# Optimization experiments

Measured on AMD Instinct MI355X. Metric: run time of the kernel, lower is better.

The kernel has to match this reference:

```python
import jax, jax.numpy as jnp
import numpy as np

HEIGHT = 32
SIGMA = 2.0
NUM_NEGATIVE = 4096
N, C = 32, 512
L = HEIGHT * HEIGHT


def _grid_weight(height: int, sigma: float) -> jnp.ndarray:
    # distance_weights: pairwise Euclidean distance between grid points
    ii, jj = np.meshgrid(np.arange(height), np.arange(height), indexing='ij')
    coords = np.stack([ii.ravel(), jj.ravel()], axis=1).astype(np.float32)  # [L, 2]
    d2 = ((coords[:, None, :] - coords[None, :, :]) ** 2).sum(-1)  # squared dist [L, L]
    w = -(0.5 / sigma ** 2) * d2
    np.fill_diagonal(w, -np.inf)
    return jax.nn.softmax(jnp.asarray(w, dtype=jnp.float32), axis=1)


def setup_inputs() -> dict:
    key = jax.random.key(0)
    k1, k2 = jax.random.split(key)
    embedding = jax.random.normal(k1, (N, L, C), dtype=jnp.float32)
    weight = _grid_weight(HEIGHT, SIGMA)  # [L, L] softmax-normalized grid kernel
    neg_indices = jax.random.randint(k2, (NUM_NEGATIVE,), 0, N * L, dtype=jnp.int64)
    return {"embedding": embedding, "weight": weight, "neg_indices": neg_indices}


def reference(embedding, weight, neg_indices):
    n, l, c = embedding.shape
    # F.normalize(dim=-1), eps=1e-12
    norm = jnp.maximum(jnp.linalg.norm(embedding, axis=-1, keepdims=True), 1e-12)
    e = embedding / norm  # [N, L, C]
    # target = weight @ e  (broadcast over batch)
    target = jnp.einsum('kl,nlc->nkc', weight, e)  # [N, L, C]
    sim_pos = jnp.sum(e * target, axis=-1)  # [N, L]
    flat = e.reshape(-1, c)  # [N*L, C]
    negatives = flat[neg_indices]  # [M, C]
    sim_neg = jnp.einsum('nlc,mc->nlm', e, negatives)  # [N, L, M]
    logits = jnp.concatenate([sim_pos[..., None], sim_neg], axis=2).reshape(n * l, 1 + neg_indices.shape[0])
    # CrossEntropyLoss with target class 0, mean reduction
    loss = -jnp.mean(jax.nn.log_softmax(logits, axis=-1)[:, 0])
    return loss
```

## Files before the change

kernel.cpp:

```cpp
#include <hip/hip_runtime.h>
#include <hip/hip_bf16.h>
#include <stdint.h>

#define L_DIM 1024
#define C_DIM 512
#define CB4 256
#define N_BATCH 32
#define M_NEG 4096
#define NROWS (N_BATCH * L_DIM)

typedef float f32x4 __attribute__((ext_vector_type(4)));
typedef int i32x4 __attribute__((ext_vector_type(4)));
typedef int i32x8 __attribute__((ext_vector_type(8)));

#define E4_SCALE 32.0f
#define MX_SCALE 122
#define FMT_FP4 4

template <int GOFF>
__device__ __forceinline__ void gl_lds16(const uint8_t* g, uint8_t* l) {
  __builtin_amdgcn_global_load_lds(
      (const __attribute__((address_space(1))) void*)g,
      (__attribute__((address_space(3))) void*)l, 16, GOFF, 0);
}

__device__ __forceinline__ uint32_t fp4_enc(float x) {
  const uint32_t s = (__float_as_uint(x) >> 31) << 3;
  const float a = fabsf(x);
  uint32_t c;
  c = a < 0.25f ? 0u
    : a < 0.75f ? 1u
    : a < 1.25f ? 2u
    : a < 1.75f ? 3u
    : a < 2.5f  ? 4u
    : a < 3.5f  ? 5u
    : a < 5.0f  ? 6u : 7u;
  return s | c;
}

__device__ __forceinline__ i32x8 fp4_op(i32x4 d) {
  return __builtin_shufflevector(d, d, 0, 1, 2, 3, -1, -1, -1, -1);
}

__device__ __forceinline__ int swz(int row) { return (row >> 1) & 3; }

__global__ __launch_bounds__(256) void k_normalize(const float* __restrict__ emb,
                                                   uint8_t* __restrict__ out,
                                                   float* __restrict__ zerobuf,
                                                   float* __restrict__ loss_out) {
  if (blockIdx.x < 1152) zerobuf[blockIdx.x * 256 + threadIdx.x] = 0.0f;
  if (blockIdx.x == 0 && threadIdx.x == 0) loss_out[0] = 0.0f;
  const int lane = threadIdx.x & 63;
  const int wave = threadIdx.x >> 6;
  const long row = (long)blockIdx.x * 4 + wave;
  const float4* src = (const float4*)(emb + row * C_DIM);
  float4 v0 = src[2 * lane];
  float4 v1 = src[2 * lane + 1];
  float ss = v0.x * v0.x + v0.y * v0.y + v0.z * v0.z + v0.w * v0.w +
             v1.x * v1.x + v1.y * v1.y + v1.z * v1.z + v1.w * v1.w;
#pragma unroll
  for (int off = 1; off < 64; off <<= 1) ss += __shfl_xor(ss, off, 64);
  const float s = E4_SCALE / fmaxf(sqrtf(ss), 1e-12f);
  uint32_t pk = fp4_enc(v0.x * s)        | (fp4_enc(v0.y * s) << 4) |
                (fp4_enc(v0.z * s) << 8) | (fp4_enc(v0.w * s) << 12) |
                (fp4_enc(v1.x * s) << 16)| (fp4_enc(v1.y * s) << 20) |
                (fp4_enc(v1.z * s) << 24)| (fp4_enc(v1.w * s) << 28);
  ((uint32_t*)(out + row * CB4))[lane] = pk;
}

__global__ __launch_bounds__(256, 4) void k_gemm_fused(
    const uint8_t* __restrict__ E4, const int* __restrict__ idx,
    const float* __restrict__ W, float* __restrict__ rowsum8,
    float* __restrict__ simpos) {
  __shared__ __align__(16) unsigned char smem_raw[40960];

  const int tid = threadIdx.x;
  const int lane = tid & 63;
  const int wave = tid >> 6;
  const int wm = wave >> 1, wn = wave & 1;
  const int q = lane >> 4, c16 = lane & 15;

  const int bid = blockIdx.x;

  if (bid < 1024) {
    uint8_t* sN = (uint8_t*)smem_raw;
    uint8_t* sE = sN + 32768;
    const int xcd = bid & 7, slot = bid >> 3;
    const long negBase = (long)(slot & 31) * 128;
    const long eBase0 = (long)(xcd * 4 + (slot >> 5)) * 1024;
    float* myrs = rowsum8 + (long)xcd * NROWS;

    const uint8_t* pN[2];
#pragma unroll
    for (int r = 0; r < 2; ++r) {
      const int c = r * 256 + tid;
      const int rw = c >> 2, cb = c & 3;
      pN[r] = E4 + (long)idx[negBase + rw] * CB4 + (cb ^ swz(rw)) * 16;
    }
    gl_lds16<0>(pN[0], sN + tid * 16);
    gl_lds16<0>(pN[1], sN + (256 + tid) * 16);
    gl_lds16<64>(pN[0], sN + 8192 + tid * 16);
    gl_lds16<64>(pN[1], sN + 8192 + (256 + tid) * 16);
    gl_lds16<128>(pN[0], sN + 16384 + tid * 16);
    gl_lds16<128>(pN[1], sN + 16384 + (256 + tid) * 16);
    gl_lds16<192>(pN[0], sN + 24576 + tid * 16);
    gl_lds16<192>(pN[1], sN + 24576 + (256 + tid) * 16);

    const uint8_t* pE[2];
#pragma unroll
    for (int r = 0; r < 2; ++r) {
      const int c = r * 256 + tid;
      const int rw = c >> 2, cb = c & 3;
      pE[r] = E4 + (eBase0 + rw) * CB4 + (cb ^ swz(rw)) * 16;
    }

    int ldsN[4], ldsE[4];
#pragma unroll
    for (int j = 0; j < 4; ++j) {
      const int rowN = wm * 64 + j * 16 + c16;
      ldsN[j] = rowN * 64 + (q ^ swz(rowN)) * 16;
      const int rowE = wn * 64 + j * 16 + c16;
      ldsE[j] = rowE * 64 + (q ^ swz(rowE)) * 16;
    }

    for (int et = 0; et < 8; ++et) {
      f32x4 acc[4][4] = {};
      auto kstep = [&](int ks) {
        __syncthreads();
        i32x8 efr[4];
#pragma unroll
        for (int j = 0; j < 4; ++j)
          efr[j] = fp4_op(*(const i32x4*)(sE + ldsE[j]));
#pragma unroll
        for (int i = 0; i < 4; ++i) {
          i32x8 nf = fp4_op(*(const i32x4*)(sN + ks * 8192 + ldsN[i]));
#pragma unroll
          for (int j = 0; j < 4; ++j)
            acc[i][j] = __builtin_amdgcn_mfma_scale_f32_16x16x128_f8f6f4(
                nf, efr[j], acc[i][j], FMT_FP4, FMT_FP4,
                0, MX_SCALE, 0, MX_SCALE);
        }
        __syncthreads();
      };
      gl_lds16<0>(pE[0], sE + tid * 16);
      gl_lds16<0>(pE[1], sE + (256 + tid) * 16);
      kstep(0);
      gl_lds16<64>(pE[0], sE + tid * 16);
      gl_lds16<64>(pE[1], sE + (256 + tid) * 16);
      kstep(1);
      gl_lds16<128>(pE[0], sE + tid * 16);
      gl_lds16<128>(pE[1], sE + (256 + tid) * 16);
      kstep(2);
      gl_lds16<192>(pE[0], sE + tid * 16);
      gl_lds16<192>(pE[1], sE + (256 + tid) * 16);
      kstep(3);
      pE[0] += 32768;
      pE[1] += 32768;

      const long eCol = eBase0 + (long)et * 128 + wn * 64 + c16;
#pragma unroll
      for (int j = 0; j < 4; ++j) {
        float s = 0.0f;
#pragma unroll
        for (int i = 0; i < 4; ++i)
#pragma unroll
          for (int r = 0; r < 4; ++r) s += __expf(acc[i][j][r]);
        s += __shfl_xor(s, 16, 64);
        s += __shfl_xor(s, 32, 64);
        if (q == 0) atomicAdd(&myrs[eCol + j * 16], s);
      }
    }
  } else {
    uint8_t* sA = (uint8_t*)smem_raw;
    uint8_t* sB = sA + 8192;
    const int t = bid - 1024;
    const int xcd = t & 7, slot = t >> 3;
    const long n = xcd * 4 + (slot & 3);
    const int inner = slot >> 2;
    const long rowBase = (long)(inner & 7) * 128;
    const long colBase = (long)(inner >> 3) * 128;
    const long aBase = n * L_DIM + rowBase;

    const uint8_t* pA[2];
    const uint8_t* pB[2];
#pragma unroll
    for (int r = 0; r < 2; ++r) {
      const int c = r * 256 + tid;
      const int rw = c >> 2, cb = c & 3;
      pA[r] = E4 + (aBase + rw) * CB4 + (cb ^ swz(rw)) * 16;
      pB[r] = E4 + (n * L_DIM + colBase + rw) * CB4 + (cb ^ swz(rw)) * 16;
    }
    int ldsB[4], ldsA[4];
#pragma unroll
    for (int j = 0; j < 4; ++j) {
      const int rowB = wn * 64 + j * 16 + c16;
      ldsB[j] = rowB * 64 + (q ^ swz(rowB)) * 16;
      const int rowA = wm * 64 + j * 16 + c16;
      ldsA[j] = rowA * 64 + (q ^ swz(rowA)) * 16;
    }

    f32x4 acc[4][4] = {};
    auto kstep = [&]() {
      __syncthreads();
      i32x8 bfr[4];
#pragma unroll
      for (int j = 0; j < 4; ++j)
        bfr[j] = fp4_op(*(const i32x4*)(sB + ldsB[j]));
#pragma unroll
      for (int i = 0; i < 4; ++i) {
        i32x8 af = fp4_op(*(const i32x4*)(sA + ldsA[i]));
#pragma unroll
        for (int j = 0; j < 4; ++j)
          acc[i][j] = __builtin_amdgcn_mfma_scale_f32_16x16x128_f8f6f4(
              af, bfr[j], acc[i][j], FMT_FP4, FMT_FP4,
              0, MX_SCALE, 0, MX_SCALE);
      }
      __syncthreads();
    };
    gl_lds16<0>(pA[0], sA + tid * 16);
    gl_lds16<0>(pA[1], sA + (256 + tid) * 16);
    gl_lds16<0>(pB[0], sB + tid * 16);
    gl_lds16<0>(pB[1], sB + (256 + tid) * 16);
    kstep();
    gl_lds16<64>(pA[0], sA + tid * 16);
    gl_lds16<64>(pA[1], sA + (256 + tid) * 16);
    gl_lds16<64>(pB[0], sB + tid * 16);
    gl_lds16<64>(pB[1], sB + (256 + tid) * 16);
    kstep();
    gl_lds16<128>(pA[0], sA + tid * 16);
    gl_lds16<128>(pA[1], sA + (256 + tid) * 16);
    gl_lds16<128>(pB[0], sB + tid * 16);
    gl_lds16<128>(pB[1], sB + (256 + tid) * 16);
    kstep();
    gl_lds16<192>(pA[0], sA + tid * 16);
    gl_lds16<192>(pA[1], sA + (256 + tid) * 16);
    gl_lds16<192>(pB[0], sB + tid * 16);
    gl_lds16<192>(pB[1], sB + (256 + tid) * 16);
    kstep();

    float* G = (float*)smem_raw;
#pragma unroll
    for (int p = 0; p < 4; ++p) {
      if (wm == (p >> 1)) {
#pragma unroll
        for (int ii = 0; ii < 2; ++ii) {
          const int i = (p & 1) * 2 + ii;
#pragma unroll
          for (int j = 0; j < 4; ++j)
#pragma unroll
            for (int r = 0; r < 4; ++r)
              G[(ii * 16 + q * 4 + r) * 132 + wn * 64 + j * 16 + c16] =
                  acc[i][j][r];
        }
      }
      __syncthreads();
      {
        const int rr = tid >> 3;
        const int chunk = tid & 7;
        const long krow = rowBase + p * 32 + rr;
        float v = 0.0f;
#pragma unroll
        for (int u = 0; u < 4; ++u) {
          const float4 g = *(const float4*)(G + rr * 132 + chunk * 16 + u * 4);
          const float4 w4 = *(const float4*)(W + krow * L_DIM + colBase +
                                             chunk * 16 + u * 4);
          v += g.x * w4.x + g.y * w4.y + g.z * w4.z + g.w * w4.w;
        }
        v += __shfl_xor(v, 1, 64);
        v += __shfl_xor(v, 2, 64);
        v += __shfl_xor(v, 4, 64);
        if (chunk == 0) atomicAdd(&simpos[n * L_DIM + krow], v);
      }
      __syncthreads();
    }
  }
}

__global__ __launch_bounds__(256) void k_finalize(const float* __restrict__ rowsum8,
                                                  const float* __restrict__ simpos,
                                                  float* __restrict__ out) {
  const int gid = blockIdx.x * 256 + threadIdx.x;
  float rs = 0.0f;
#pragma unroll
  for (int x = 0; x < 8; ++x) rs += rowsum8[x * NROWS + gid];
  const float sp = simpos[gid];
  float v = __logf(rs + __expf(sp)) - sp;
#pragma unroll
  for (int off = 1; off < 64; off <<= 1) v += __shfl_xor(v, off, 64);
  __shared__ float ws[4];
  if ((threadIdx.x & 63) == 0) ws[threadIdx.x >> 6] = v;
  __syncthreads();
  if (threadIdx.x == 0)
    atomicAdd(out, (ws[0] + ws[1] + ws[2] + ws[3]) * (1.0f / (float)NROWS));
}

extern "C" void kernel_launch(void* const* d_in, const int* in_sizes, int n_in,
                              void* d_out, int out_size, void* d_ws, size_t ws_size,
                              hipStream_t stream) {
  const float* emb = (const float*)d_in[0];
  const float* weight = (const float*)d_in[1];
  const int* negidx = (const int*)d_in[2];
  float* out = (float*)d_out;
  char* ws = (char*)d_ws;

  uint8_t* E4 = (uint8_t*)ws;
  float* rowsum8 = (float*)(ws + 8388608);
  float* simpos = (float*)(ws + 9437184);

  k_normalize<<<NROWS / 4, 256, 0, stream>>>(emb, E4, rowsum8, out);
  k_gemm_fused<<<3072, 256, 0, stream>>>(E4, negidx, weight, rowsum8, simpos);
  k_finalize<<<NROWS / 256, 256, 0, stream>>>(rowsum8, simpos, out);
}
```

Measured before the change: 190.6 us.

## Swap stationary operand in negative GEMM and reduce row sums in registers

After: 176.8 us. -7.2%, faster.

```diff
diff --git a/kernel.cpp b/kernel.cpp
--- a/kernel.cpp
+++ b/kernel.cpp
@@ -46,9 +46,9 @@
 
 __global__ __launch_bounds__(256) void k_normalize(const float* __restrict__ emb,
                                                    uint8_t* __restrict__ out,
-                                                   float* __restrict__ zerobuf,
+                                                   float* __restrict__ simpos,
                                                    float* __restrict__ loss_out) {
-  if (blockIdx.x < 1152) zerobuf[blockIdx.x * 256 + threadIdx.x] = 0.0f;
+  if (blockIdx.x < 128) simpos[blockIdx.x * 256 + threadIdx.x] = 0.0f;
   if (blockIdx.x == 0 && threadIdx.x == 0) loss_out[0] = 0.0f;
   const int lane = threadIdx.x & 63;
   const int wave = threadIdx.x >> 6;
@@ -70,7 +70,7 @@
 
 __global__ __launch_bounds__(256, 4) void k_gemm_fused(
     const uint8_t* __restrict__ E4, const int* __restrict__ idx,
-    const float* __restrict__ W, float* __restrict__ rowsum8,
+    const float* __restrict__ W, float* __restrict__ rowsum4,
     float* __restrict__ simpos) {
   __shared__ __align__(16) unsigned char smem_raw[40960];
 
@@ -83,92 +83,119 @@
   const int bid = blockIdx.x;
 
   if (bid < 1024) {
-    uint8_t* sN = (uint8_t*)smem_raw;
-    uint8_t* sE = sN + 32768;
-    const int xcd = bid & 7, slot = bid >> 3;
-    const long negBase = (long)(slot & 31) * 128;
-    const long eBase0 = (long)(xcd * 4 + (slot >> 5)) * 1024;
-    float* myrs = rowsum8 + (long)xcd * NROWS;
-
-    const uint8_t* pN[2];
-#pragma unroll
-    for (int r = 0; r < 2; ++r) {
-      const int c = r * 256 + tid;
-      const int rw = c >> 2, cb = c & 3;
-      pN[r] = E4 + (long)idx[negBase + rw] * CB4 + (cb ^ swz(rw)) * 16;
-    }
-    gl_lds16<0>(pN[0], sN + tid * 16);
-    gl_lds16<0>(pN[1], sN + (256 + tid) * 16);
-    gl_lds16<64>(pN[0], sN + 8192 + tid * 16);
-    gl_lds16<64>(pN[1], sN + 8192 + (256 + tid) * 16);
-    gl_lds16<128>(pN[0], sN + 16384 + tid * 16);
-    gl_lds16<128>(pN[1], sN + 16384 + (256 + tid) * 16);
-    gl_lds16<192>(pN[0], sN + 24576 + tid * 16);
-    gl_lds16<192>(pN[1], sN + 24576 + (256 + tid) * 16);
-
-    const uint8_t* pE[2];
-#pragma unroll
-    for (int r = 0; r < 2; ++r) {
-      const int c = r * 256 + tid;
-      const int rw = c >> 2, cb = c & 3;
-      pE[r] = E4 + (eBase0 + rw) * CB4 + (cb ^ swz(rw)) * 16;
-    }
-
-    int ldsN[4], ldsE[4];
+    uint8_t* sE = (uint8_t*)smem_raw;
+    uint8_t* sN = sE + 32768;
+    const int xcd = bid & 7, s = bid >> 3;
+    const int negQ = s & 3;
+    const long eBase = ((long)xcd * 32 + (s >> 2)) * 128;
+    const int negBase = negQ * 1024;
+
+    {
+      const uint8_t* pE[2];
+#pragma unroll
+      for (int r = 0; r < 2; ++r) {
+        const int c = r * 256 + tid;
+        const int rw = c >> 2, cb = c & 3;
+        pE[r] = E4 + (eBase + rw) * CB4 + (cb ^ swz(rw)) * 16;
+      }
+      gl_lds16<0>(pE[0], sE + tid * 16);
+      gl_lds16<0>(pE[1], sE + (256 + tid) * 16);
+      gl_lds16<64>(pE[0], sE + 8192 + tid * 16);
+      gl_lds16<64>(pE[1], sE + 8192 + (256 + tid) * 16);
+      gl_lds16<128>(pE[0], sE + 16384 + tid * 16);
+      gl_lds16<128>(pE[1], sE + 16384 + (256 + tid) * 16);
+      gl_lds16<192>(pE[0], sE + 24576 + tid * 16);
+      gl_lds16<192>(pE[1], sE + 24576 + (256 + tid) * 16);
+    }
+
+    const int rw0 = tid >> 2, cb0 = tid & 3;
+    const int c1 = 256 + tid;
+    const int rw1 = c1 >> 2, cb1 = c1 & 3;
+    const int off0 = (cb0 ^ swz(rw0)) * 16;
+    const int off1 = (cb1 ^ swz(rw1)) * 16;
+    const int* ip0 = idx + negBase + rw0;
+    const int* ip1 = idx + negBase + rw1;
+
+    int ldsA[4], ldsB[4];
 #pragma unroll
     for (int j = 0; j < 4; ++j) {
-      const int rowN = wm * 64 + j * 16 + c16;
-      ldsN[j] = rowN * 64 + (q ^ swz(rowN)) * 16;
-      const int rowE = wn * 64 + j * 16 + c16;
-      ldsE[j] = rowE * 64 + (q ^ swz(rowE)) * 16;
-    }
-
-    for (int et = 0; et < 8; ++et) {
+      const int rowA = wm * 64 + j * 16 + c16;
+      ldsA[j] = rowA * 64 + (q ^ swz(rowA)) * 16;
+      const int rowB = wn * 64 + j * 16 + c16;
+      ldsB[j] = rowB * 64 + (q ^ swz(rowB)) * 16;
+    }
+
+    float s16[16];
+#pragma unroll
+    for (int v = 0; v < 16; ++v) s16[v] = 0.0f;
+
+    for (int t = 0; t < 8; ++t) {
+      const uint8_t* q0 = E4 + (long)ip0[t * 128] * CB4 + off0;
+      const uint8_t* q1 = E4 + (long)ip1[t * 128] * CB4 + off1;
       f32x4 acc[4][4] = {};
       auto kstep = [&](int ks) {
         __syncthreads();
-        i32x8 efr[4];
+        i32x8 bfr[4];
 #pragma unroll
         for (int j = 0; j < 4; ++j)
-          efr[j] = fp4_op(*(const i32x4*)(sE + ldsE[j]));
+          bfr[j] = fp4_op(*(const i32x4*)(sN + ldsB[j]));
 #pragma unroll
         for (int i = 0; i < 4; ++i) {
-          i32x8 nf = fp4_op(*(const i32x4*)(sN + ks * 8192 + ldsN[i]));
+          i32x8 af = fp4_op(*(const i32x4*)(sE + ks * 8192 + ldsA[i]));
 #pragma unroll
           for (int j = 0; j < 4; ++j)
             acc[i][j] = __builtin_amdgcn_mfma_scale_f32_16x16x128_f8f6f4(
-                nf, efr[j], acc[i][j], FMT_FP4, FMT_FP4,
+                af, bfr[j], acc[i][j], FMT_FP4, FMT_FP4,
                 0, MX_SCALE, 0, MX_SCALE);
         }
         __syncthreads();
       };
-      gl_lds16<0>(pE[0], sE + tid * 16);
-      gl_lds16<0>(pE[1], sE + (256 + tid) * 16);
+      gl_lds16<0>(q0, sN + tid * 16);
+      gl_lds16<0>(q1, sN + (256 + tid) * 16);
       kstep(0);
-      gl_lds16<64>(pE[0], sE + tid * 16);
-      gl_lds16<64>(pE[1], sE + (256 + tid) * 16);
+      gl_lds16<64>(q0, sN + tid * 16);
+      gl_lds16<64>(q1, sN + (256 + tid) * 16);
       kstep(1);
-      gl_lds16<128>(pE[0], sE + tid * 16);
-      gl_lds16<128>(pE[1], sE + (256 + tid) * 16);
+      gl_lds16<128>(q0, sN + tid * 16);
+      gl_lds16<128>(q1, sN + (256 + tid) * 16);
       kstep(2);
-      gl_lds16<192>(pE[0], sE + tid * 16);
-      gl_lds16<192>(pE[1], sE + (256 + tid) * 16);
+      gl_lds16<192>(q0, sN + tid * 16);
+      gl_lds16<192>(q1, sN + (256 + tid) * 16);
       kstep(3);
-      pE[0] += 32768;
-      pE[1] += 32768;
-
-      const long eCol = eBase0 + (long)et * 128 + wn * 64 + c16;
-#pragma unroll
-      for (int j = 0; j < 4; ++j) {
-        float s = 0.0f;
-#pragma unroll
-        for (int i = 0; i < 4; ++i)
-#pragma unroll
-          for (int r = 0; r < 4; ++r) s += __expf(acc[i][j][r]);
-        s += __shfl_xor(s, 16, 64);
-        s += __shfl_xor(s, 32, 64);
-        if (q == 0) atomicAdd(&myrs[eCol + j * 16], s);
-      }
+
+#pragma unroll
+      for (int i = 0; i < 4; ++i)
+#pragma unroll
+        for (int r = 0; r < 4; ++r)
+          s16[i * 4 + r] += __expf(acc[i][0][r]) + __expf(acc[i][1][r]) +
+                            __expf(acc[i][2][r]) + __expf(acc[i][3][r]);
+    }
+
+#pragma unroll
+    for (int v = 0; v < 16; ++v) {
+      s16[v] += __shfl_xor(s16[v], 1, 64);
+      s16[v] += __shfl_xor(s16[v], 2, 64);
+      s16[v] += __shfl_xor(s16[v], 4, 64);
+      s16[v] += __shfl_xor(s16[v], 8, 64);
+    }
+    float* red = (float*)sN;
+    if (wn == 1 && c16 == 0) {
+#pragma unroll
+      for (int i = 0; i < 4; ++i)
+#pragma unroll
+        for (int r = 0; r < 4; ++r)
+          red[wm * 64 + i * 16 + q * 4 + r] = s16[i * 4 + r];
+    }
+    __syncthreads();
+    if (wn == 0 && c16 == 0) {
+      float* dst = rowsum4 + (long)negQ * NROWS + eBase;
+#pragma unroll
+      for (int i = 0; i < 4; ++i)
+#pragma unroll
+        for (int r = 0; r < 4; ++r) {
+          const int row = wm * 64 + i * 16 + q * 4 + r;
+          dst[row] = s16[i * 4 + r] + red[row];
+        }
     }
   } else {
     uint8_t* sA = (uint8_t*)smem_raw;
@@ -276,13 +303,12 @@
   }
 }
 
-__global__ __launch_bounds__(256) void k_finalize(const float* __restrict__ rowsum8,
+__global__ __launch_bounds__(256) void k_finalize(const float* __restrict__ rowsum4,
                                                   const float* __restrict__ simpos,
                                                   float* __restrict__ out) {
   const int gid = blockIdx.x * 256 + threadIdx.x;
-  float rs = 0.0f;
-#pragma unroll
-  for (int x = 0; x < 8; ++x) rs += rowsum8[x * NROWS + gid];
+  const float rs = rowsum4[gid] + rowsum4[NROWS + gid] +
+                   rowsum4[2 * NROWS + gid] + rowsum4[3 * NROWS + gid];
   const float sp = simpos[gid];
   float v = __logf(rs + __expf(sp)) - sp;
 #pragma unroll
@@ -304,10 +330,10 @@
   char* ws = (char*)d_ws;
 
   uint8_t* E4 = (uint8_t*)ws;
-  float* rowsum8 = (float*)(ws + 8388608);
-  float* simpos = (float*)(ws + 9437184);
-
-  k_normalize<<<NROWS / 4, 256, 0, stream>>>(emb, E4, rowsum8, out);
-  k_gemm_fused<<<3072, 256, 0, stream>>>(E4, negidx, weight, rowsum8, simpos);
-  k_finalize<<<NROWS / 256, 256, 0, stream>>>(rowsum8, simpos, out);
-}
+  float* rowsum4 = (float*)(ws + 8388608);
+  float* simpos = (float*)(ws + 8912896);
+
+  k_normalize<<<NROWS / 4, 256, 0, stream>>>(emb, E4, simpos, out);
+  k_gemm_fused<<<3072, 256, 0, stream>>>(E4, negidx, weight, rowsum4, simpos);
+  k_finalize<<<NROWS / 256, 256, 0, stream>>>(rowsum4, simpos, out);
+}
```
